# Optimization experiments

Measured on AMD Instinct MI355X. Metric: run time of the kernel, lower is better.

Reference implementation:

```python
import jax, jax.numpy as jnp
import numpy as np

B, T, E, D, OUT = 2048, 64, 256, 256, 2


def setup_inputs() -> dict:
    key = jax.random.key(0)
    ks = jax.random.split(key, 16)
    s = 0.05
    return {
        "input_encoded": jax.random.normal(ks[0], (B, T, E), dtype=jnp.float32),
        "y_history": jax.random.normal(ks[1], (B, T), dtype=jnp.float32),
        # attn_layer: Linear(2D+E -> E), Tanh, Linear(E -> 1)
        "W1": jax.random.normal(ks[2], (E, 2 * D + E), dtype=jnp.float32) * s,
        "b1": jax.random.normal(ks[3], (E,), dtype=jnp.float32) * s,
        "w2": jax.random.normal(ks[4], (E,), dtype=jnp.float32) * s,
        "b2": jax.random.normal(ks[5], (1,), dtype=jnp.float32) * s,
        # single-layer LSTM(input=OUT, hidden=D); gate order i,f,g,o
        "W_ih": jax.random.normal(ks[6], (4 * D, OUT), dtype=jnp.float32) * s,
        "b_ih": jax.random.normal(ks[7], (4 * D,), dtype=jnp.float32) * s,
        "W_hh": jax.random.normal(ks[8], (4 * D, D), dtype=jnp.float32) * s,
        "b_hh": jax.random.normal(ks[9], (4 * D,), dtype=jnp.float32) * s,
        # fc: Linear(E+T -> OUT) (torch init normal_() std=1; scaled here for stability)
        "W_fc": jax.random.normal(ks[10], (OUT, E + T), dtype=jnp.float32) * s,
        "b_fc": jax.random.normal(ks[11], (OUT,), dtype=jnp.float32) * s,
        # fc_final: Linear(D+E -> OUT)
        "W_final": jax.random.normal(ks[12], (OUT, D + E), dtype=jnp.float32) * s,
        "b_final": jax.random.normal(ks[13], (OUT,), dtype=jnp.float32) * s,
    }


def reference(input_encoded, y_history, W1, b1, w2, b2, W_ih, b_ih, W_hh, b_hh,
              W_fc, b_fc, W_final, b_final):
    Bs, Ts, Es = input_encoded.shape
    Ds = W_hh.shape[1]

    def step(carry, _):
        h, c, _ctx = carry  # h, c: [B, D]
        hc = jnp.concatenate([h, c], axis=-1)  # [B, 2D]
        hc_rep = jnp.broadcast_to(hc[:, None, :], (Bs, Ts, 2 * Ds))
        x = jnp.concatenate([hc_rep, input_encoded], axis=-1)  # [B, T, 2D+E]
        scores = jnp.tanh(x @ W1.T + b1) @ w2 + b2  # [B, T]
        alpha = jax.nn.softmax(scores, axis=1)
        ctx = jnp.einsum('bt,bte->be', alpha, input_encoded)  # [B, E]
        y_tilde = jnp.concatenate([ctx, y_history], axis=1) @ W_fc.T + b_fc  # [B, OUT]
        gates = y_tilde @ W_ih.T + b_ih + h @ W_hh.T + b_hh  # [B, 4D]
        i, f, g, o = jnp.split(gates, 4, axis=-1)
        c_new = jax.nn.sigmoid(f) * c + jax.nn.sigmoid(i) * jnp.tanh(g)
        h_new = jax.nn.sigmoid(o) * jnp.tanh(c_new)
        return (h_new, c_new, ctx), None

    init = (jnp.zeros((Bs, Ds), input_encoded.dtype),
            jnp.zeros((Bs, Ds), input_encoded.dtype),
            jnp.zeros((Bs, Es), input_encoded.dtype))
    (h, c, ctx), _ = jax.lax.scan(step, init, None, length=Ts)
    return jnp.concatenate([h, ctx], axis=1) @ W_final.T + b_final  # [B, OUT]
```

## Files before the change

kernel.cpp:

```cpp
#include <hip/hip_runtime.h>
#include <hip/hip_bf16.h>
#include <cstdint>
#include <cstddef>

#define LOG2E 1.44269504088896340736f

using f32x4 = __attribute__((ext_vector_type(4))) float;
using s16x8 = __attribute__((ext_vector_type(8))) short;

static __device__ __forceinline__ float bf2f(unsigned short u) {
  union { unsigned int i; float f; } v; v.i = ((unsigned int)u) << 16; return v.f;
}
static __device__ __forceinline__ unsigned short f2bf(float f) {
  union { float f; unsigned int i; } v; v.f = f;
  unsigned int r = v.i + 0x7fffu + ((v.i >> 16) & 1u);
  return (unsigned short)(r >> 16);
}
static __device__ __forceinline__ float wredmax(float v) {
  #pragma unroll
  for (int m = 32; m > 0; m >>= 1) v = fmaxf(v, __shfl_xor(v, m, 64));
  return v;
}
static __device__ __forceinline__ float wredsum(float v) {
  #pragma unroll
  for (int m = 32; m > 0; m >>= 1) v += __shfl_xor(v, m, 64);
  return v;
}

__global__ void ktrans(const float* __restrict__ W1, const float* __restrict__ b1,
                       const float* __restrict__ Wih_in, const float* __restrict__ bih,
                       const float* __restrict__ Whh, const float* __restrict__ bhh,
                       const float* __restrict__ Wfc, const float* __restrict__ bfc,
                       const float* __restrict__ yhist,
                       unsigned short* __restrict__ WB1, unsigned short* __restrict__ WBhh,
                       unsigned short* __restrict__ WB1e, float* __restrict__ b1s,
                       float* __restrict__ Wihs, float* __restrict__ gbias,
                       float* __restrict__ yh2)
{
  int idx = blockIdx.x * 256 + threadIdx.x;
  const float TS = 2.f * LOG2E;
  if (idx < 131072) {
    int k = idx >> 8, e = idx & 255;
    WB1[((k >> 3) * 256 + e) * 8 + (k & 7)] = f2bf(TS * W1[e * 768 + k]);
    return;
  }
  idx -= 131072;
  if (idx < 262144) {
    int k = idx >> 10, j = idx & 1023;
    float sc = ((j >> 8) == 2) ? TS : -LOG2E;
    WBhh[((k >> 3) * 1024 + j) * 8 + (k & 7)] = f2bf(sc * Whh[j * 256 + k]);
    return;
  }
  idx -= 262144;
  if (idx < 65536) {
    int k = idx >> 8, e = idx & 255;
    WB1e[((k >> 3) * 256 + e) * 8 + (k & 7)] = f2bf(TS * W1[e * 768 + 512 + k]);
    return;
  }
  idx -= 65536;
  if (idx < 256) { b1s[idx] = TS * b1[idx]; return; }
  idx -= 256;
  if (idx < 2048) {
    int j = idx >> 1;
    float sc = ((j >> 8) == 2) ? TS : -LOG2E;
    Wihs[idx] = sc * Wih_in[idx];
    return;
  }
  idx -= 2048;
  if (idx < 1024) {
    int j = idx;
    float sc = ((j >> 8) == 2) ? TS : -LOG2E;
    gbias[j] = sc * (bih[j] + bhh[j]);
    return;
  }
  idx -= 1024;
  if (idx < 4096) {
    int bq = idx >> 1, o = idx & 1;
    float a = bfc[o];
    for (int t = 0; t < 64; ++t) a = fmaf(yhist[bq * 64 + t], Wfc[o * 320 + 256 + t], a);
    yh2[idx] = a;
    return;
  }
}

__global__ __launch_bounds__(256, 4) void kpre(
    const float* __restrict__ x, const unsigned short* __restrict__ WB1e,
    const float* __restrict__ Wfc,
    unsigned short* __restrict__ P, float* __restrict__ ey)
{
  __shared__ __align__(16) unsigned short xs[16384];
  const int bq = blockIdx.x;
  const int tid = threadIdx.x;
  const int w = tid >> 6, lane = tid & 63;
  const float* __restrict__ xb = x + (size_t)bq * 16384;

  #pragma unroll 4
  for (int it = 0; it < 16; ++it) {
    int idx = it * 256 + tid;
    float4 v = *(const float4*)(xb + (size_t)idx * 4);
    int t = idx >> 6, e0 = (idx & 63) * 4;
    unsigned long long pk = (unsigned long long)f2bf(v.x)
        | ((unsigned long long)f2bf(v.y) << 16)
        | ((unsigned long long)f2bf(v.z) << 32)
        | ((unsigned long long)f2bf(v.w) << 48);
    int ba = (t * 512 + e0 * 2) ^ ((t & 7) << 4);
    *(unsigned long long*)((char*)xs + ba) = pk;
  }
  __syncthreads();

  const int mt = w;
  const int fgrp = lane >> 4, fcol = lane & 15;
  const int trow = mt * 16 + fcol;
  s16x8 af[8];
  #pragma unroll
  for (int kb = 0; kb < 8; ++kb) {
    int e = kb * 32 + fgrp * 8;
    int ba = (trow * 512 + e * 2) ^ ((trow & 7) << 4);
    af[kb] = *(const s16x8*)((char*)xs + ba);
  }
  __syncthreads();

  unsigned short* __restrict__ Pst = xs;
  #pragma unroll
  for (int nt = 0; nt < 16; ++nt) {
    s16x8 bfr[8];
    #pragma unroll
    for (int kb = 0; kb < 8; ++kb)
      bfr[kb] = *(const s16x8*)&WB1e[(size_t)((kb * 4 + fgrp) * 256 + nt * 16 + fcol) * 8];
    f32x4 acc = {0.f, 0.f, 0.f, 0.f};
    #pragma unroll
    for (int kb = 0; kb < 8; ++kb)
      acc = __builtin_amdgcn_mfma_f32_16x16x32_bf16(af[kb], bfr[kb], acc, 0, 0, 0);
    const int ep = nt * 16 + fcol;
    #pragma unroll
    for (int r = 0; r < 4; ++r)
      Pst[(mt * 16 + fgrp * 4 + r) * 256 + ep] = f2bf(acc[r]);
  }
  __syncthreads();

  unsigned int* __restrict__ Pd = (unsigned int*)(P + (size_t)bq * 16384);
  #pragma unroll 4
  for (int d = tid; d < 8192; d += 256) {
    int f = d * 2;
    int ec = f >> 9, t = (f >> 3) & 63, i0 = f & 7;
    unsigned int lo = Pst[t * 256 + ec * 8 + i0];
    unsigned int hi = Pst[t * 256 + ec * 8 + i0 + 1];
    Pd[d] = lo | (hi << 16);
  }

  if (tid < 128) {
    int t = tid >> 1, o = tid & 1;
    float a = 0.f;
    const float* __restrict__ xr = xb + t * 256;
    const float* __restrict__ wr = Wfc + o * 320;
    #pragma unroll 4
    for (int e = 0; e < 256; ++e) a = fmaf(xr[e], wr[e], a);
    ey[((size_t)bq * 64 + t) * 2 + o] = a;
  }
}

#define SIG(X) __builtin_amdgcn_rcpf(1.f + __builtin_amdgcn_exp2f(X))

#define SCCHUNK(PV, U) do { \
  const float4 qa_ = *(const float4*)(qrowh + (U) * 8); \
  const float4 qc_ = *(const float4*)(qrowh + (U) * 8 + 4); \
  const float4 wa_ = *(const float4*)(w2h + (U) * 8); \
  const float4 wc_ = *(const float4*)(w2h + (U) * 8 + 4); \
  a0 = fmaf(wa_.x, SIG(bf2f((unsigned short)(PV)[0]) + qa_.x), a0); \
  a1 = fmaf(wa_.y, SIG(bf2f((unsigned short)(PV)[1]) + qa_.y), a1); \
  a2 = fmaf(wa_.z, SIG(bf2f((unsigned short)(PV)[2]) + qa_.z), a2); \
  a3 = fmaf(wa_.w, SIG(bf2f((unsigned short)(PV)[3]) + qa_.w), a3); \
  a0 = fmaf(wc_.x, SIG(bf2f((unsigned short)(PV)[4]) + qc_.x), a0); \
  a1 = fmaf(wc_.y, SIG(bf2f((unsigned short)(PV)[5]) + qc_.y), a1); \
  a2 = fmaf(wc_.z, SIG(bf2f((unsigned short)(PV)[6]) + qc_.z), a2); \
  a3 = fmaf(wc_.w, SIG(bf2f((unsigned short)(PV)[7]) + qc_.w), a3); \
} while (0)

#define AHF(KB) (*(const s16x8*)&hcA[(((KB) * 4 + fgrp) * 8 + frow) * 8])

#define GUNIT4(GG) do { \
  const int jg_ = (GG) * 256 + wv * 16 + fcol; \
  const size_t jb_ = (size_t)jg_ * 8; \
  const s16x8 wb0_ = *(const s16x8*)&WBhh[jb_ + (size_t)(0 * 4 + fgrp) * 8192]; \
  const s16x8 wb1_ = *(const s16x8*)&WBhh[jb_ + (size_t)(1 * 4 + fgrp) * 8192]; \
  const s16x8 wb2_ = *(const s16x8*)&WBhh[jb_ + (size_t)(2 * 4 + fgrp) * 8192]; \
  const s16x8 wb3_ = *(const s16x8*)&WBhh[jb_ + (size_t)(3 * 4 + fgrp) * 8192]; \
  const s16x8 wb4_ = *(const s16x8*)&WBhh[jb_ + (size_t)(4 * 4 + fgrp) * 8192]; \
  const s16x8 wb5_ = *(const s16x8*)&WBhh[jb_ + (size_t)(5 * 4 + fgrp) * 8192]; \
  const s16x8 wb6_ = *(const s16x8*)&WBhh[jb_ + (size_t)(6 * 4 + fgrp) * 8192]; \
  const s16x8 wb7_ = *(const s16x8*)&WBhh[jb_ + (size_t)(7 * 4 + fgrp) * 8192]; \
  const float gbj_ = gbS[jg_]; \
  GA##GG = (f32x4){gbj_, gbj_, gbj_, gbj_}; \
  GA##GG = __builtin_amdgcn_mfma_f32_16x16x32_bf16(AHF(0), wb0_, GA##GG, 0, 0, 0); \
  GA##GG = __builtin_amdgcn_mfma_f32_16x16x32_bf16(AHF(1), wb1_, GA##GG, 0, 0, 0); \
  GA##GG = __builtin_amdgcn_mfma_f32_16x16x32_bf16(AHF(2), wb2_, GA##GG, 0, 0, 0); \
  GA##GG = __builtin_amdgcn_mfma_f32_16x16x32_bf16(AHF(3), wb3_, GA##GG, 0, 0, 0); \
  GA##GG = __builtin_amdgcn_mfma_f32_16x16x32_bf16(AHF(4), wb4_, GA##GG, 0, 0, 0); \
  GA##GG = __builtin_amdgcn_mfma_f32_16x16x32_bf16(AHF(5), wb5_, GA##GG, 0, 0, 0); \
  GA##GG = __builtin_amdgcn_mfma_f32_16x16x32_bf16(AHF(6), wb6_, GA##GG, 0, 0, 0); \
  GA##GG = __builtin_amdgcn_mfma_f32_16x16x32_bf16(AHF(7), wb7_, GA##GG, 0, 0, 0); \
} while (0)

#define PWR(R, CV) do { \
  const int row_ = drow0 + (R); \
  const float y0_ = yt[row_][0], y1_ = yt[row_][1]; \
  const float gi_ = GA0[R] + fmaf(wI0, y0_, wI1 * y1_); \
  const float gf_ = GA1[R] + fmaf(wF0, y0_, wF1 * y1_); \
  const float gg_ = GA2[R] + fmaf(wG0, y0_, wG1 * y1_); \
  const float go_ = GA3[R] + fmaf(wO0, y0_, wO1 * y1_); \
  const float si_ = SIG(gi_); \
  const float sf_ = SIG(gf_); \
  const float tg_ = 1.f - 2.f * SIG(gg_); \
  const float so_ = SIG(go_); \
  const float cn_ = sf_ * (CV) + si_ * tg_; \
  (CV) = cn_; \
  const float th_ = 1.f - 2.f * SIG(2.f * LOG2E * cn_); \
  const float hn_ = so_ * th_; \
  hcA[((jj >> 3) * 8 + row_) * 8 + (jj & 7)] = f2bf(hn_); \
  hcA[((32 + (jj >> 3)) * 8 + row_) * 8 + (jj & 7)] = f2bf(cn_); \
  if (s == 63) hF[row_][jj] = hn_; \
} while (0)

#define PLOADR(U) const s16x8 p##U = *(const s16x8*)(Pb + (U) * 512 + lane * 8);

__global__
__attribute__((amdgpu_flat_work_group_size(1024, 1024), amdgpu_waves_per_eu(4, 4)))
void krecur(
    const float* __restrict__ x, const float* __restrict__ w2g,
    const unsigned short* __restrict__ WB1, const unsigned short* __restrict__ WBhh,
    const float* __restrict__ Wihs, const float* __restrict__ gbias,
    const float* __restrict__ b1s, const float* __restrict__ yh2,
    const float* __restrict__ ey, const unsigned short* __restrict__ P,
    const float* __restrict__ Wfin, const float* __restrict__ bfin,
    float* __restrict__ out)
{
  __shared__ __align__(16) unsigned short hcA[4096];
  __shared__ __align__(16) float qf[8][256];
  __shared__ __align__(16) float w2f[256];
  __shared__ __align__(16) float ps[8][2][64];
  __shared__ __align__(16) float scAl[8][64];
  __shared__ float yt[8][2];
  __shared__ __align__(16) float wi0S[1024];
  __shared__ __align__(16) float wi1S[1024];
  __shared__ __align__(16) float gbS[1024];
  __shared__ __align__(16) float hF[8][256];
  __shared__ __align__(16) float ctxS[8][256];

  const int tid = threadIdx.x;
  const int wv = tid >> 6, lane = tid & 63;
  const int row = wv >> 1, half = wv & 1;
  const int gbase = blockIdx.x * 8;
  const int gb = gbase + row;

  for (int i = tid; i < 4096; i += 1024) hcA[i] = 0;
  if (tid < 256) w2f[tid] = w2g[tid];
  wi0S[tid] = Wihs[2 * tid];
  wi1S[tid] = Wihs[2 * tid + 1];
  gbS[tid]  = gbias[tid];

  const int frow = lane & 7;
  const int fgrp = lane >> 4;
  const int fcol = lane & 15;
  const int drow0 = fgrp * 4;

  const unsigned short* __restrict__ Pb = P + (size_t)gb * 16384 + (size_t)half * 8192;
  PLOADR(0)  PLOADR(1)  PLOADR(2)  PLOADR(3)
  PLOADR(4)  PLOADR(5)  PLOADR(6)  PLOADR(7)
  PLOADR(8)  PLOADR(9)  PLOADR(10) PLOADR(11)
  PLOADR(12) PLOADR(13) PLOADR(14) PLOADR(15)

  const float2 eyv = *(const float2*)(ey + ((size_t)gb * 64 + lane) * 2);
  const float yh0 = yh2[gb * 2], yh1 = yh2[gb * 2 + 1];
  const float b1r = b1s[wv * 16 + fcol];

  float c0 = 0.f, c1 = 0.f, c2 = 0.f, c3 = 0.f;

  __syncthreads();

  for (int s = 0; s < 64; ++s) {
    {
      f32x4 acc = {0.f, 0.f, 0.f, 0.f};
      #pragma unroll
      for (int kb = 0; kb < 16; ++kb) {
        const s16x8 bfr = *(const s16x8*)&WB1[(size_t)((kb * 4 + fgrp) * 256 + wv * 16 + fcol) * 8];
        acc = __builtin_amdgcn_mfma_f32_16x16x32_bf16(AHF(kb), bfr, acc, 0, 0, 0);
      }
      if (lane < 32) {
        #pragma unroll
        for (int r = 0; r < 4; ++r) qf[drow0 + r][wv * 16 + fcol] = acc[r] + b1r;
      }
    }
    __syncthreads();

    {
      const float* __restrict__ qrowh = &qf[row][0] + half * 128;
      const float* __restrict__ w2h = w2f + half * 128;
      float a0 = 0.f, a1 = 0.f, a2 = 0.f, a3 = 0.f;
      SCCHUNK(p0, 0);   SCCHUNK(p1, 1);   SCCHUNK(p2, 2);   SCCHUNK(p3, 3);
      SCCHUNK(p4, 4);   SCCHUNK(p5, 5);   SCCHUNK(p6, 6);   SCCHUNK(p7, 7);
      SCCHUNK(p8, 8);   SCCHUNK(p9, 9);   SCCHUNK(p10, 10); SCCHUNK(p11, 11);
      SCCHUNK(p12, 12); SCCHUNK(p13, 13); SCCHUNK(p14, 14); SCCHUNK(p15, 15);
      ps[row][half][lane] = (a0 + a1) + (a2 + a3);
    }
    __syncthreads();

    f32x4 GA0, GA1, GA2, GA3;
    GUNIT4(0); GUNIT4(1); GUNIT4(2); GUNIT4(3);
    {
      float sc = -2.f * (ps[row][0][lane] + ps[row][1][lane]);
      float mx = wredmax(sc);
      float e_t = __builtin_amdgcn_exp2f((sc - mx) * LOG2E);
      float sm = wredsum(e_t);
      float alpha = e_t * __builtin_amdgcn_rcpf(sm);
      if (s == 63 && half == 0) scAl[row][lane] = alpha;
      float y0 = wredsum(alpha * eyv.x);
      float y1 = wredsum(alpha * eyv.y);
      if (half == 0 && lane == 0) { yt[row][0] = y0 + yh0; yt[row][1] = y1 + yh1; }
    }
    __syncthreads();

    if (lane < 32) {
      const int jj = wv * 16 + fcol;
      const float wI0 = wi0S[jj],       wI1 = wi1S[jj];
      const float wF0 = wi0S[256 + jj], wF1 = wi1S[256 + jj];
      const float wG0 = wi0S[512 + jj], wG1 = wi1S[512 + jj];
      const float wO0 = wi0S[768 + jj], wO1 = wi1S[768 + jj];
      PWR(0, c0); PWR(1, c1); PWR(2, c2); PWR(3, c3);
    }
    __syncthreads();

    if (s == 63) {
      #pragma unroll
      for (int pp = 0; pp < 2; ++pp) {
        const int e = (half * 2 + pp) * 64 + lane;
        float a = 0.f;
        const float* __restrict__ xr = x + (size_t)gb * 16384 + e;
        #pragma unroll 8
        for (int t = 0; t < 64; ++t) a = fmaf(scAl[row][t], xr[t * 256], a);
        ctxS[row][e] = a;
      }
      __syncthreads();
    }
  }

  if (half == 0) {
    float o0 = 0.f, o1 = 0.f;
    #pragma unroll
    for (int kk = 0; kk < 8; ++kk) {
      const int k = kk * 64 + lane;
      const float v = (k < 256) ? hF[row][k] : ctxS[row][k - 256];
      o0 = fmaf(v, Wfin[k], o0);
      o1 = fmaf(v, Wfin[512 + k], o1);
    }
    o0 = wredsum(o0);
    o1 = wredsum(o1);
    if (lane == 0) {
      out[gb * 2 + 0] = o0 + bfin[0];
      out[gb * 2 + 1] = o1 + bfin[1];
    }
  }
}

extern "C" void kernel_launch(void* const* d_in, const int* in_sizes, int n_in,
                              void* d_out, int out_size, void* d_ws, size_t ws_size,
                              hipStream_t stream) {
  const float* x    = (const float*)d_in[0];
  const float* yh   = (const float*)d_in[1];
  const float* W1   = (const float*)d_in[2];
  const float* b1   = (const float*)d_in[3];
  const float* w2   = (const float*)d_in[4];
  const float* Wih  = (const float*)d_in[6];
  const float* bih  = (const float*)d_in[7];
  const float* Whh  = (const float*)d_in[8];
  const float* bhh  = (const float*)d_in[9];
  const float* Wfc  = (const float*)d_in[10];
  const float* bfc  = (const float*)d_in[11];
  const float* Wfin = (const float*)d_in[12];
  const float* bfin = (const float*)d_in[13];

  char* ws = (char*)d_ws;
  unsigned short* P    = (unsigned short*)(ws + 0);
  unsigned short* WB1  = (unsigned short*)(ws + 67108864);
  unsigned short* WBhh = (unsigned short*)(ws + 67371008);
  unsigned short* WB1e = (unsigned short*)(ws + 67895296);
  float* b1s   = (float*)(ws + 68026368);
  float* Wihs  = (float*)(ws + 68027392);
  float* gbias = (float*)(ws + 68035584);
  float* yh2   = (float*)(ws + 68039680);
  float* ey    = (float*)(ws + 68056064);

  ktrans<<<1821, 256, 0, stream>>>(W1, b1, Wih, bih, Whh, bhh, Wfc, bfc, yh,
                                   WB1, WBhh, WB1e, b1s, Wihs, gbias, yh2);
  kpre<<<2048, 256, 0, stream>>>(x, WB1e, Wfc, P, ey);
  krecur<<<256, 1024, 0, stream>>>(x, w2, WB1, WBhh, Wihs, gbias, b1s, yh2, ey, P,
                                   Wfin, bfin, (float*)d_out);
}
```

Measured before the change: 4.571 ms.

## Stage half of P tile in LDS, keep LSTM weights in registers

Moves the upper half of each row's precomputed P chunks (8 of 16 s16x8 vectors per lane) from registers into a 128KB LDS buffer, reusing that buffer afterwards for hF/ctxS. The LSTM input weights and gate biases now live in registers instead of LDS. The W_hh MFMA loop is reordered so each A fragment from LDS is loaded once and reused across four gates. It also drops the waves_per_eu(4,4) attribute in favour of launch_bounds(1024). The aim is to cut register pressure and avoid spills, at the cost of extra LDS reads every step and a large LDS footprint.

```diff
diff --git a/kernel.cpp b/kernel.cpp
--- a/kernel.cpp
+++ b/kernel.cpp
@@ -176,30 +176,12 @@
   a3 = fmaf(wc_.w, SIG(bf2f((unsigned short)(PV)[7]) + qc_.w), a3); \
 } while (0)
 
+#define SCL(U) do { \
+  const s16x8 pvL_ = *(const s16x8*)&Pl[row][half][(U) - 8][lane][0]; \
+  SCCHUNK(pvL_, U); \
+} while (0)
+
 #define AHF(KB) (*(const s16x8*)&hcA[(((KB) * 4 + fgrp) * 8 + frow) * 8])
-
-#define GUNIT4(GG) do { \
-  const int jg_ = (GG) * 256 + wv * 16 + fcol; \
-  const size_t jb_ = (size_t)jg_ * 8; \
-  const s16x8 wb0_ = *(const s16x8*)&WBhh[jb_ + (size_t)(0 * 4 + fgrp) * 8192]; \
-  const s16x8 wb1_ = *(const s16x8*)&WBhh[jb_ + (size_t)(1 * 4 + fgrp) * 8192]; \
-  const s16x8 wb2_ = *(const s16x8*)&WBhh[jb_ + (size_t)(2 * 4 + fgrp) * 8192]; \
-  const s16x8 wb3_ = *(const s16x8*)&WBhh[jb_ + (size_t)(3 * 4 + fgrp) * 8192]; \
-  const s16x8 wb4_ = *(const s16x8*)&WBhh[jb_ + (size_t)(4 * 4 + fgrp) * 8192]; \
-  const s16x8 wb5_ = *(const s16x8*)&WBhh[jb_ + (size_t)(5 * 4 + fgrp) * 8192]; \
-  const s16x8 wb6_ = *(const s16x8*)&WBhh[jb_ + (size_t)(6 * 4 + fgrp) * 8192]; \
-  const s16x8 wb7_ = *(const s16x8*)&WBhh[jb_ + (size_t)(7 * 4 + fgrp) * 8192]; \
-  const float gbj_ = gbS[jg_]; \
-  GA##GG = (f32x4){gbj_, gbj_, gbj_, gbj_}; \
-  GA##GG = __builtin_amdgcn_mfma_f32_16x16x32_bf16(AHF(0), wb0_, GA##GG, 0, 0, 0); \
-  GA##GG = __builtin_amdgcn_mfma_f32_16x16x32_bf16(AHF(1), wb1_, GA##GG, 0, 0, 0); \
-  GA##GG = __builtin_amdgcn_mfma_f32_16x16x32_bf16(AHF(2), wb2_, GA##GG, 0, 0, 0); \
-  GA##GG = __builtin_amdgcn_mfma_f32_16x16x32_bf16(AHF(3), wb3_, GA##GG, 0, 0, 0); \
-  GA##GG = __builtin_amdgcn_mfma_f32_16x16x32_bf16(AHF(4), wb4_, GA##GG, 0, 0, 0); \
-  GA##GG = __builtin_amdgcn_mfma_f32_16x16x32_bf16(AHF(5), wb5_, GA##GG, 0, 0, 0); \
-  GA##GG = __builtin_amdgcn_mfma_f32_16x16x32_bf16(AHF(6), wb6_, GA##GG, 0, 0, 0); \
-  GA##GG = __builtin_amdgcn_mfma_f32_16x16x32_bf16(AHF(7), wb7_, GA##GG, 0, 0, 0); \
-} while (0)
 
 #define PWR(R, CV) do { \
   const int row_ = drow0 + (R); \
@@ -216,16 +198,14 @@
   (CV) = cn_; \
   const float th_ = 1.f - 2.f * SIG(2.f * LOG2E * cn_); \
   const float hn_ = so_ * th_; \
-  hcA[((jj >> 3) * 8 + row_) * 8 + (jj & 7)] = f2bf(hn_); \
-  hcA[((32 + (jj >> 3)) * 8 + row_) * 8 + (jj & 7)] = f2bf(cn_); \
-  if (s == 63) hF[row_][jj] = hn_; \
+  hcA[((jj0 >> 3) * 8 + row_) * 8 + (jj0 & 7)] = f2bf(hn_); \
+  hcA[((32 + (jj0 >> 3)) * 8 + row_) * 8 + (jj0 & 7)] = f2bf(cn_); \
+  if (s == 63) hF[row_ * 256 + jj0] = hn_; \
 } while (0)
 
-#define PLOADR(U) const s16x8 p##U = *(const s16x8*)(Pb + (U) * 512 + lane * 8);
-
-__global__
-__attribute__((amdgpu_flat_work_group_size(1024, 1024), amdgpu_waves_per_eu(4, 4)))
-void krecur(
+#define PLOADR(U) const s16x8 p##U = *(const s16x8*)(Pb + (size_t)(U) * 512 + lane * 8);
+
+__global__ __launch_bounds__(1024) void krecur(
     const float* __restrict__ x, const float* __restrict__ w2g,
     const unsigned short* __restrict__ WB1, const unsigned short* __restrict__ WBhh,
     const float* __restrict__ Wihs, const float* __restrict__ gbias,
@@ -234,17 +214,16 @@
     const float* __restrict__ Wfin, const float* __restrict__ bfin,
     float* __restrict__ out)
 {
+  __shared__ __align__(16) unsigned short Pl[8][2][8][64][8];
   __shared__ __align__(16) unsigned short hcA[4096];
   __shared__ __align__(16) float qf[8][256];
   __shared__ __align__(16) float w2f[256];
   __shared__ __align__(16) float ps[8][2][64];
   __shared__ __align__(16) float scAl[8][64];
   __shared__ float yt[8][2];
-  __shared__ __align__(16) float wi0S[1024];
-  __shared__ __align__(16) float wi1S[1024];
-  __shared__ __align__(16) float gbS[1024];
-  __shared__ __align__(16) float hF[8][256];
-  __shared__ __align__(16) float ctxS[8][256];
+
+  float* const hF   = (float*)&Pl[0][0][0][0][0];
+  float* const ctxS = hF + 2048;
 
   const int tid = threadIdx.x;
   const int wv = tid >> 6, lane = tid & 63;
@@ -254,9 +233,12 @@
 
   for (int i = tid; i < 4096; i += 1024) hcA[i] = 0;
   if (tid < 256) w2f[tid] = w2g[tid];
-  wi0S[tid] = Wihs[2 * tid];
-  wi1S[tid] = Wihs[2 * tid + 1];
-  gbS[tid]  = gbias[tid];
+  for (int i = tid; i < 8192; i += 1024) {
+    int rw = i >> 10, rem = i & 1023;
+    int hf = rem >> 9, ch = (rem >> 6) & 7, t = rem & 63;
+    *(s16x8*)&Pl[rw][hf][ch][t][0] =
+        *(const s16x8*)(P + (size_t)(gbase + rw) * 16384 + (size_t)(hf * 16 + 8 + ch) * 512 + t * 8);
+  }
 
   const int frow = lane & 7;
   const int fgrp = lane >> 4;
@@ -264,14 +246,19 @@
   const int drow0 = fgrp * 4;
 
   const unsigned short* __restrict__ Pb = P + (size_t)gb * 16384 + (size_t)half * 8192;
-  PLOADR(0)  PLOADR(1)  PLOADR(2)  PLOADR(3)
-  PLOADR(4)  PLOADR(5)  PLOADR(6)  PLOADR(7)
-  PLOADR(8)  PLOADR(9)  PLOADR(10) PLOADR(11)
-  PLOADR(12) PLOADR(13) PLOADR(14) PLOADR(15)
+  PLOADR(0) PLOADR(1) PLOADR(2) PLOADR(3)
+  PLOADR(4) PLOADR(5) PLOADR(6) PLOADR(7)
 
   const float2 eyv = *(const float2*)(ey + ((size_t)gb * 64 + lane) * 2);
   const float yh0 = yh2[gb * 2], yh1 = yh2[gb * 2 + 1];
-  const float b1r = b1s[wv * 16 + fcol];
+  const int jj0 = wv * 16 + fcol;
+  const float b1r = b1s[jj0];
+  const float wI0 = Wihs[2 * jj0],          wI1 = Wihs[2 * jj0 + 1];
+  const float wF0 = Wihs[2 * (256 + jj0)],  wF1 = Wihs[2 * (256 + jj0) + 1];
+  const float wG0 = Wihs[2 * (512 + jj0)],  wG1 = Wihs[2 * (512 + jj0) + 1];
+  const float wO0 = Wihs[2 * (768 + jj0)],  wO1 = Wihs[2 * (768 + jj0) + 1];
+  const float gb_0 = gbias[jj0],       gb_1 = gbias[256 + jj0];
+  const float gb_2 = gbias[512 + jj0], gb_3 = gbias[768 + jj0];
 
   float c0 = 0.f, c1 = 0.f, c2 = 0.f, c3 = 0.f;
 
@@ -282,12 +269,13 @@
       f32x4 acc = {0.f, 0.f, 0.f, 0.f};
       #pragma unroll
       for (int kb = 0; kb < 16; ++kb) {
-        const s16x8 bfr = *(const s16x8*)&WB1[(size_t)((kb * 4 + fgrp) * 256 + wv * 16 + fcol) * 8];
-        acc = __builtin_amdgcn_mfma_f32_16x16x32_bf16(AHF(kb), bfr, acc, 0, 0, 0);
+        const s16x8 a_ = AHF(kb);
+        const s16x8 b_ = *(const s16x8*)&WB1[(size_t)((kb * 4 + fgrp) * 256 + jj0) * 8];
+        acc = __builtin_amdgcn_mfma_f32_16x16x32_bf16(a_, b_, acc, 0, 0, 0);
       }
       if (lane < 32) {
         #pragma unroll
-        for (int r = 0; r < 4; ++r) qf[drow0 + r][wv * 16 + fcol] = acc[r] + b1r;
+        for (int r = 0; r < 4; ++r) qf[drow0 + r][jj0] = acc[r] + b1r;
       }
     }
     __syncthreads();
@@ -296,16 +284,30 @@
       const float* __restrict__ qrowh = &qf[row][0] + half * 128;
       const float* __restrict__ w2h = w2f + half * 128;
       float a0 = 0.f, a1 = 0.f, a2 = 0.f, a3 = 0.f;
-      SCCHUNK(p0, 0);   SCCHUNK(p1, 1);   SCCHUNK(p2, 2);   SCCHUNK(p3, 3);
-      SCCHUNK(p4, 4);   SCCHUNK(p5, 5);   SCCHUNK(p6, 6);   SCCHUNK(p7, 7);
-      SCCHUNK(p8, 8);   SCCHUNK(p9, 9);   SCCHUNK(p10, 10); SCCHUNK(p11, 11);
-      SCCHUNK(p12, 12); SCCHUNK(p13, 13); SCCHUNK(p14, 14); SCCHUNK(p15, 15);
+      SCCHUNK(p0, 0); SCCHUNK(p1, 1); SCCHUNK(p2, 2); SCCHUNK(p3, 3);
+      SCCHUNK(p4, 4); SCCHUNK(p5, 5); SCCHUNK(p6, 6); SCCHUNK(p7, 7);
+      SCL(8); SCL(9); SCL(10); SCL(11); SCL(12); SCL(13); SCL(14); SCL(15);
       ps[row][half][lane] = (a0 + a1) + (a2 + a3);
     }
     __syncthreads();
 
-    f32x4 GA0, GA1, GA2, GA3;
-    GUNIT4(0); GUNIT4(1); GUNIT4(2); GUNIT4(3);
+    f32x4 GA0 = {gb_0, gb_0, gb_0, gb_0};
+    f32x4 GA1 = {gb_1, gb_1, gb_1, gb_1};
+    f32x4 GA2 = {gb_2, gb_2, gb_2, gb_2};
+    f32x4 GA3 = {gb_3, gb_3, gb_3, gb_3};
+    #pragma unroll
+    for (int kb = 0; kb < 8; ++kb) {
+      const s16x8 a_ = AHF(kb);
+      const size_t ko_ = (size_t)(kb * 4 + fgrp) * 8192;
+      const s16x8 b0_ = *(const s16x8*)&WBhh[ko_ + (size_t)(jj0) * 8];
+      const s16x8 b1_ = *(const s16x8*)&WBhh[ko_ + (size_t)(256 + jj0) * 8];
+      const s16x8 b2_ = *(const s16x8*)&WBhh[ko_ + (size_t)(512 + jj0) * 8];
+      const s16x8 b3_ = *(const s16x8*)&WBhh[ko_ + (size_t)(768 + jj0) * 8];
+      GA0 = __builtin_amdgcn_mfma_f32_16x16x32_bf16(a_, b0_, GA0, 0, 0, 0);
+      GA1 = __builtin_amdgcn_mfma_f32_16x16x32_bf16(a_, b1_, GA1, 0, 0, 0);
+      GA2 = __builtin_amdgcn_mfma_f32_16x16x32_bf16(a_, b2_, GA2, 0, 0, 0);
+      GA3 = __builtin_amdgcn_mfma_f32_16x16x32_bf16(a_, b3_, GA3, 0, 0, 0);
+    }
     {
       float sc = -2.f * (ps[row][0][lane] + ps[row][1][lane]);
       float mx = wredmax(sc);
@@ -320,11 +322,6 @@
     __syncthreads();
 
     if (lane < 32) {
-      const int jj = wv * 16 + fcol;
-      const float wI0 = wi0S[jj],       wI1 = wi1S[jj];
-      const float wF0 = wi0S[256 + jj], wF1 = wi1S[256 + jj];
-      const float wG0 = wi0S[512 + jj], wG1 = wi1S[512 + jj];
-      const float wO0 = wi0S[768 + jj], wO1 = wi1S[768 + jj];
       PWR(0, c0); PWR(1, c1); PWR(2, c2); PWR(3, c3);
     }
     __syncthreads();
@@ -337,7 +334,7 @@
         const float* __restrict__ xr = x + (size_t)gb * 16384 + e;
         #pragma unroll 8
         for (int t = 0; t < 64; ++t) a = fmaf(scAl[row][t], xr[t * 256], a);
-        ctxS[row][e] = a;
+        ctxS[row * 256 + e] = a;
       }
       __syncthreads();
     }
@@ -348,7 +345,7 @@
     #pragma unroll
     for (int kk = 0; kk < 8; ++kk) {
       const int k = kk * 64 + lane;
-      const float v = (k < 256) ? hF[row][k] : ctxS[row][k - 256];
+      const float v = (k < 256) ? hF[row * 256 + k] : ctxS[row * 256 + (k - 256)];
       o0 = fmaf(v, Wfin[k], o0);
       o1 = fmaf(v, Wfin[512 + k], o1);
     }
```

New measurement: 3.910 ms. -14.5%, faster.
